# Kernel tuning notes

Hardware: AMD Instinct MI355X
Metric: run time of the kernel (lower is better)

The kernel has to match this reference:

```python
import jax, jax.numpy as jnp
import numpy as np

COMMITMENT_COST = 0.25
NUM_EMBEDDINGS = 512
EMBEDDING_DIM = 64


def setup_inputs() -> dict:
    key = jax.random.key(0)
    k1, k2 = jax.random.split(key)
    inputs = jax.random.normal(k1, (64, EMBEDDING_DIM, 32, 32), dtype=jnp.float32)
    # nn.Embedding init: uniform(-1/K, 1/K)
    emb_w = jax.random.uniform(
        k2, (NUM_EMBEDDINGS, EMBEDDING_DIM), dtype=jnp.float32,
        minval=-1.0 / NUM_EMBEDDINGS, maxval=1.0 / NUM_EMBEDDINGS)
    return {"inputs": inputs, "emb_w": emb_w}


def reference(inputs, emb_w):
    sg = jax.lax.stop_gradient
    # NCHW -> NHWC
    x = jnp.transpose(inputs, (0, 2, 3, 1))          # [B, H, W, D]
    B, H, W, D = x.shape
    flat = x.reshape(-1, D)                          # [N, D]
    dist = (jnp.sum(flat * flat, axis=1, keepdims=True)
            + jnp.sum(emb_w * emb_w, axis=1)
            - 2.0 * jnp.dot(flat, emb_w.T))          # [N, K]
    idx = jnp.argmin(dist, axis=1)                   # [N]
    # one-hot @ emb_w is just a gather
    quantized = emb_w[idx].reshape(B, H, W, D)       # [B, H, W, D]
    e_latent_loss = jnp.mean((sg(quantized) - x) ** 2)
    q_latent_loss = jnp.mean((quantized - sg(x)) ** 2)
    loss = q_latent_loss + COMMITMENT_COST * e_latent_loss
    # straight-through estimator
    quantized_st = x + sg(quantized - x)
    out = jnp.transpose(quantized_st, (0, 3, 1, 2))  # back to NCHW
    return loss, out, idx[:, None]
```

## Files before the change

### kernel.cpp

```cpp
#include <hip/hip_runtime.h>


#define D_    64
#define HW_   1024
#define N_    65536
#define K_    512
#define M_    128
#define CH_   128
#define NCH_  4
#define NDTOT (N_ * D_)

__global__ __launch_bounds__(256) void vq_norm_kernel(const float* __restrict__ emb,
                                                      float* __restrict__ wsn) {
    int k = blockIdx.x * 256 + threadIdx.x;
    if (k < K_) {
        const float* e = emb + k * D_;
        float r[8];
#pragma unroll
        for (int j = 0; j < 8; ++j) r[j] = __fmul_rn(e[j], e[j]);
#pragma unroll
        for (int i = 1; i < 8; ++i)
#pragma unroll
            for (int j = 0; j < 8; ++j)
                r[j] = __fadd_rn(r[j], __fmul_rn(e[i * 8 + j], e[i * 8 + j]));
        float s = __fadd_rn(__fadd_rn(__fadd_rn(r[0], r[1]), __fadd_rn(r[2], r[3])),
                            __fadd_rn(__fadd_rn(r[4], r[5]), __fadd_rn(r[6], r[7])));
        wsn[k] = s;
    }
}

__global__ __launch_bounds__(256, 2) void vq_main_kernel(const float* __restrict__ inp,
                                                         const float* __restrict__ emb,
                                                         const float* __restrict__ wsn,
                                                         float* __restrict__ out) {
    __shared__ float lds[16520];
    float* ldsx = lds;
    float* ldse = lds + 8192;
    float* sxs  = lds + 16384;
    float* partial = lds + 16512;

    const int tid = threadIdx.x;
    const int pg  = tid & 15;
    const int kg  = tid >> 4;
    const int n0  = blockIdx.x * M_;
    const int b   = n0 >> 10;
    const int hw0 = n0 & 1023;
    const float* xbase = inp + b * (D_ * HW_) + hw0;

#pragma unroll
    for (int i = 0; i < 8; ++i) {
        int q  = i * 256 + tid;
        int d  = q >> 5;
        int pq = q & 31;
        float4 v = *(const float4*)(xbase + d * HW_ + pq * 4);
        *(float4*)(ldsx + d * M_ + pq * 4) = v;
    }
    __syncthreads();

    if (tid < M_) {
        float r[8];
#pragma unroll
        for (int j = 0; j < 8; ++j) {
            float v = ldsx[j * M_ + tid];
            r[j] = __fmul_rn(v, v);
        }
#pragma unroll
        for (int i = 1; i < 8; ++i)
#pragma unroll
            for (int j = 0; j < 8; ++j) {
                float v = ldsx[(i * 8 + j) * M_ + tid];
                r[j] = __fadd_rn(r[j], __fmul_rn(v, v));
            }
        sxs[tid] = __fadd_rn(__fadd_rn(__fadd_rn(r[0], r[1]), __fadd_rn(r[2], r[3])),
                             __fadd_rn(__fadd_rn(r[4], r[5]), __fadd_rn(r[6], r[7])));
    }
    __syncthreads();

    float sxp[8];
#pragma unroll
    for (int pp = 0; pp < 8; ++pp) sxp[pp] = sxs[pg * 8 + pp];

    float runv[8];
    int   runi[8];
#pragma unroll
    for (int pp = 0; pp < 8; ++pp) { runv[pp] = 3.4e38f; runi[pp] = 0; }

    for (int c = 0; c < NCH_; ++c) {
        __syncthreads();
#pragma unroll
        for (int i = 0; i < 8; ++i) {
            int q  = i * 256 + tid;
            int kl = q & 127;
            int dq = q >> 7;
            float4 v = *(const float4*)(emb + (c * CH_ + kl) * D_ + dq * 4);
            ldse[(dq * 4 + 0) * CH_ + kl] = v.x;
            ldse[(dq * 4 + 1) * CH_ + kl] = v.y;
            ldse[(dq * 4 + 2) * CH_ + kl] = v.z;
            ldse[(dq * 4 + 3) * CH_ + kl] = v.w;
        }
        float4 nh0 = *(const float4*)(wsn + c * CH_ + kg * 8);
        float4 nh1 = *(const float4*)(wsn + c * CH_ + kg * 8 + 4);
        __syncthreads();

        float acc[8][8];
#pragma unroll
        for (int pp = 0; pp < 8; ++pp)
#pragma unroll
            for (int kk = 0; kk < 8; ++kk) acc[pp][kk] = 0.f;

#pragma unroll 2
        for (int d = 0; d < D_; ++d) {
            float4 xa = *(const float4*)(ldsx + d * M_ + pg * 8);
            float4 xb = *(const float4*)(ldsx + d * M_ + pg * 8 + 4);
            float4 ea = *(const float4*)(ldse + d * CH_ + kg * 8);
            float4 eb = *(const float4*)(ldse + d * CH_ + kg * 8 + 4);
            float xr[8] = {xa.x, xa.y, xa.z, xa.w, xb.x, xb.y, xb.z, xb.w};
            float er[8] = {ea.x, ea.y, ea.z, ea.w, eb.x, eb.y, eb.z, eb.w};
#pragma unroll
            for (int pp = 0; pp < 8; ++pp)
#pragma unroll
                for (int kk = 0; kk < 8; ++kk)
                    acc[pp][kk] = fmaf(xr[pp], er[kk], acc[pp][kk]);
        }

        float nk[8] = {nh0.x, nh0.y, nh0.z, nh0.w, nh1.x, nh1.y, nh1.z, nh1.w};
#pragma unroll
        for (int pp = 0; pp < 8; ++pp) {
            float sx = sxp[pp];
#pragma unroll
            for (int kk = 0; kk < 8; ++kk) {
                float t1 = __fadd_rn(sx, nk[kk]);
                float v  = __fadd_rn(t1, -2.0f * acc[pp][kk]);
                if (v < runv[pp]) { runv[pp] = v; runi[pp] = c * CH_ + kg * 8 + kk; }
            }
        }
    }

    __syncthreads();
    float* sv = ldse;
    int*   si = (int*)(ldse + 2048);
    int*   fi = (int*)(ldse + 4096);
#pragma unroll
    for (int pp = 0; pp < 8; ++pp) {
        sv[kg * M_ + pg * 8 + pp] = runv[pp];
        si[kg * M_ + pg * 8 + pp] = runi[pp];
    }
    __syncthreads();
    if (tid < M_) {
        float bv = 3.4e38f; int bi = 0x7fffffff;
#pragma unroll
        for (int g = 0; g < 16; ++g) {
            float v  = sv[g * M_ + tid];
            int   ii = si[g * M_ + tid];
            if (v < bv || (v == bv && ii < bi)) { bv = v; bi = ii; }
        }
        fi[tid] = bi;
        out[1 + NDTOT + n0 + tid] = (float)bi;
    }
    __syncthreads();

    float* obase = out + 1 + b * (D_ * HW_) + hw0;
    float local = 0.f;
    for (int i = 0; i < 32; ++i) {
        int q = i * 256 + tid;
        int d = q >> 7;
        int p = q & 127;
        int idx = fi[p];
        float e  = emb[idx * D_ + d];
        float xv = ldsx[d * M_ + p];
        float df = e - xv;
        local = fmaf(df, df, local);
        obase[d * HW_ + p] = e;
    }
#pragma unroll
    for (int off = 32; off > 0; off >>= 1)
        local += __shfl_down(local, off, 64);
    if ((tid & 63) == 0) partial[tid >> 6] = local;
    __syncthreads();
    if (tid == 0) {
        float t = partial[0] + partial[1] + partial[2] + partial[3];
        atomicAdd(out, t * (1.25f / (float)NDTOT));
    }
}

extern "C" void kernel_launch(void* const* d_in, const int* in_sizes, int n_in,
                              void* d_out, int out_size, void* d_ws, size_t ws_size,
                              hipStream_t stream) {
    const float* inp = (const float*)d_in[0];
    const float* emb = (const float*)d_in[1];
    float* out = (float*)d_out;
    float* wsn = (float*)d_ws;

    hipMemsetAsync(d_out, 0, sizeof(float), stream);
    vq_norm_kernel<<<2, 256, 0, stream>>>(emb, wsn);
    vq_main_kernel<<<512, 256, 0, stream>>>(inp, emb, wsn, out);
}
```

Before: 131.9 us.

## Fuse codebook norm into main kernel and hold pixel vectors in registers

Removes the separate norm kernel; each block now computes all codebook norms into LDS itself. The distance computation is restructured so each thread keeps two full 64-dim pixel vectors in registers and streams codebook rows directly from global memory (wave-uniform addresses), with each wave covering a quarter of the codebook. This drops the LDS staging and transpose of codebook chunks and the extra launch, at the cost of much lower per-load FMA reuse, redundant norm work per block, and high register pressure.

```diff
diff --git a/kernel.cpp b/kernel.cpp
--- a/kernel.cpp
+++ b/kernel.cpp
@@ -6,45 +6,24 @@
 #define N_    65536
 #define K_    512
 #define M_    128
-#define CH_   128
-#define NCH_  4
 #define NDTOT (N_ * D_)
 
-__global__ __launch_bounds__(256) void vq_norm_kernel(const float* __restrict__ emb,
-                                                      float* __restrict__ wsn) {
-    int k = blockIdx.x * 256 + threadIdx.x;
-    if (k < K_) {
-        const float* e = emb + k * D_;
-        float r[8];
-#pragma unroll
-        for (int j = 0; j < 8; ++j) r[j] = __fmul_rn(e[j], e[j]);
-#pragma unroll
-        for (int i = 1; i < 8; ++i)
-#pragma unroll
-            for (int j = 0; j < 8; ++j)
-                r[j] = __fadd_rn(r[j], __fmul_rn(e[i * 8 + j], e[i * 8 + j]));
-        float s = __fadd_rn(__fadd_rn(__fadd_rn(r[0], r[1]), __fadd_rn(r[2], r[3])),
-                            __fadd_rn(__fadd_rn(r[4], r[5]), __fadd_rn(r[6], r[7])));
-        wsn[k] = s;
-    }
-}
+__global__ __launch_bounds__(256, 2) void vq_fused_kernel(const float* __restrict__ inp,
+                                                          const float* __restrict__ emb,
+                                                          float* __restrict__ out) {
+    __shared__ float ldsx[D_ * M_];
+    __shared__ float ldsn[K_];
+    __shared__ float sv[4 * M_];
+    __shared__ int   si[4 * M_];
+    __shared__ int   fi[M_];
+    __shared__ float partial[4];
 
-__global__ __launch_bounds__(256, 2) void vq_main_kernel(const float* __restrict__ inp,
-                                                         const float* __restrict__ emb,
-                                                         const float* __restrict__ wsn,
-                                                         float* __restrict__ out) {
-    __shared__ float lds[16520];
-    float* ldsx = lds;
-    float* ldse = lds + 8192;
-    float* sxs  = lds + 16384;
-    float* partial = lds + 16512;
-
-    const int tid = threadIdx.x;
-    const int pg  = tid & 15;
-    const int kg  = tid >> 4;
-    const int n0  = blockIdx.x * M_;
-    const int b   = n0 >> 10;
-    const int hw0 = n0 & 1023;
+    const int tid  = threadIdx.x;
+    const int lane = tid & 63;
+    const int w    = tid >> 6;
+    const int n0   = blockIdx.x * M_;
+    const int b    = n0 >> 10;
+    const int hw0  = n0 & 1023;
     const float* xbase = inp + b * (D_ * HW_) + hw0;
 
 #pragma unroll
@@ -55,101 +34,91 @@
         float4 v = *(const float4*)(xbase + d * HW_ + pq * 4);
         *(float4*)(ldsx + d * M_ + pq * 4) = v;
     }
-    __syncthreads();
 
-    if (tid < M_) {
+#pragma unroll
+    for (int c = 0; c < 2; ++c) {
+        const int k = c * 256 + tid;
+        const float* e = emb + k * D_;
+        float el[64];
+#pragma unroll
+        for (int q = 0; q < 16; ++q) {
+            float4 v = *(const float4*)(e + q * 4);
+            el[4 * q + 0] = v.x; el[4 * q + 1] = v.y;
+            el[4 * q + 2] = v.z; el[4 * q + 3] = v.w;
+        }
         float r[8];
 #pragma unroll
-        for (int j = 0; j < 8; ++j) {
-            float v = ldsx[j * M_ + tid];
-            r[j] = __fmul_rn(v, v);
-        }
+        for (int j = 0; j < 8; ++j) r[j] = __fmul_rn(el[j], el[j]);
 #pragma unroll
         for (int i = 1; i < 8; ++i)
 #pragma unroll
-            for (int j = 0; j < 8; ++j) {
-                float v = ldsx[(i * 8 + j) * M_ + tid];
-                r[j] = __fadd_rn(r[j], __fmul_rn(v, v));
-            }
-        sxs[tid] = __fadd_rn(__fadd_rn(__fadd_rn(r[0], r[1]), __fadd_rn(r[2], r[3])),
-                             __fadd_rn(__fadd_rn(r[4], r[5]), __fadd_rn(r[6], r[7])));
+            for (int j = 0; j < 8; ++j)
+                r[j] = __fadd_rn(r[j], __fmul_rn(el[i * 8 + j], el[i * 8 + j]));
+        ldsn[k] = __fadd_rn(__fadd_rn(__fadd_rn(r[0], r[1]), __fadd_rn(r[2], r[3])),
+                            __fadd_rn(__fadd_rn(r[4], r[5]), __fadd_rn(r[6], r[7])));
     }
     __syncthreads();
 
-    float sxp[8];
+    float x0[64], x1[64];
 #pragma unroll
-    for (int pp = 0; pp < 8; ++pp) sxp[pp] = sxs[pg * 8 + pp];
-
-    float runv[8];
-    int   runi[8];
-#pragma unroll
-    for (int pp = 0; pp < 8; ++pp) { runv[pp] = 3.4e38f; runi[pp] = 0; }
-
-    for (int c = 0; c < NCH_; ++c) {
-        __syncthreads();
-#pragma unroll
-        for (int i = 0; i < 8; ++i) {
-            int q  = i * 256 + tid;
-            int kl = q & 127;
-            int dq = q >> 7;
-            float4 v = *(const float4*)(emb + (c * CH_ + kl) * D_ + dq * 4);
-            ldse[(dq * 4 + 0) * CH_ + kl] = v.x;
-            ldse[(dq * 4 + 1) * CH_ + kl] = v.y;
-            ldse[(dq * 4 + 2) * CH_ + kl] = v.z;
-            ldse[(dq * 4 + 3) * CH_ + kl] = v.w;
-        }
-        float4 nh0 = *(const float4*)(wsn + c * CH_ + kg * 8);
-        float4 nh1 = *(const float4*)(wsn + c * CH_ + kg * 8 + 4);
-        __syncthreads();
-
-        float acc[8][8];
-#pragma unroll
-        for (int pp = 0; pp < 8; ++pp)
-#pragma unroll
-            for (int kk = 0; kk < 8; ++kk) acc[pp][kk] = 0.f;
-
-#pragma unroll 2
-        for (int d = 0; d < D_; ++d) {
-            float4 xa = *(const float4*)(ldsx + d * M_ + pg * 8);
-            float4 xb = *(const float4*)(ldsx + d * M_ + pg * 8 + 4);
-            float4 ea = *(const float4*)(ldse + d * CH_ + kg * 8);
-            float4 eb = *(const float4*)(ldse + d * CH_ + kg * 8 + 4);
-            float xr[8] = {xa.x, xa.y, xa.z, xa.w, xb.x, xb.y, xb.z, xb.w};
-            float er[8] = {ea.x, ea.y, ea.z, ea.w, eb.x, eb.y, eb.z, eb.w};
-#pragma unroll
-            for (int pp = 0; pp < 8; ++pp)
-#pragma unroll
-                for (int kk = 0; kk < 8; ++kk)
-                    acc[pp][kk] = fmaf(xr[pp], er[kk], acc[pp][kk]);
-        }
-
-        float nk[8] = {nh0.x, nh0.y, nh0.z, nh0.w, nh1.x, nh1.y, nh1.z, nh1.w};
-#pragma unroll
-        for (int pp = 0; pp < 8; ++pp) {
-            float sx = sxp[pp];
-#pragma unroll
-            for (int kk = 0; kk < 8; ++kk) {
-                float t1 = __fadd_rn(sx, nk[kk]);
-                float v  = __fadd_rn(t1, -2.0f * acc[pp][kk]);
-                if (v < runv[pp]) { runv[pp] = v; runi[pp] = c * CH_ + kg * 8 + kk; }
-            }
-        }
+    for (int d = 0; d < 64; ++d) {
+        float2 v = *(const float2*)(ldsx + d * M_ + 2 * lane);
+        x0[d] = v.x; x1[d] = v.y;
     }
 
-    __syncthreads();
-    float* sv = ldse;
-    int*   si = (int*)(ldse + 2048);
-    int*   fi = (int*)(ldse + 4096);
+    float r0[8], r1[8];
 #pragma unroll
-    for (int pp = 0; pp < 8; ++pp) {
-        sv[kg * M_ + pg * 8 + pp] = runv[pp];
-        si[kg * M_ + pg * 8 + pp] = runi[pp];
+    for (int j = 0; j < 8; ++j) {
+        r0[j] = __fmul_rn(x0[j], x0[j]);
+        r1[j] = __fmul_rn(x1[j], x1[j]);
+    }
+#pragma unroll
+    for (int i = 1; i < 8; ++i)
+#pragma unroll
+        for (int j = 0; j < 8; ++j) {
+            r0[j] = __fadd_rn(r0[j], __fmul_rn(x0[i * 8 + j], x0[i * 8 + j]));
+            r1[j] = __fadd_rn(r1[j], __fmul_rn(x1[i * 8 + j], x1[i * 8 + j]));
+        }
+    const float sx0 = __fadd_rn(__fadd_rn(__fadd_rn(r0[0], r0[1]), __fadd_rn(r0[2], r0[3])),
+                                __fadd_rn(__fadd_rn(r0[4], r0[5]), __fadd_rn(r0[6], r0[7])));
+    const float sx1 = __fadd_rn(__fadd_rn(__fadd_rn(r1[0], r1[1]), __fadd_rn(r1[2], r1[3])),
+                                __fadd_rn(__fadd_rn(r1[4], r1[5]), __fadd_rn(r1[6], r1[7])));
+
+    float runv0 = 3.4e38f, runv1 = 3.4e38f;
+    int   runi0 = 0,       runi1 = 0;
+    const int k0 = w << 7;
+    const float* ew = emb + k0 * D_;
+#pragma unroll 2
+    for (int kk = 0; kk < 128; ++kk) {
+        const float* ek = ew + kk * D_;
+        const float nk = ldsn[k0 + kk];
+        float acc0 = 0.f, acc1 = 0.f;
+#pragma unroll
+        for (int q = 0; q < 16; ++q) {
+            float4 ev = *(const float4*)(ek + q * 4);
+            acc0 = fmaf(x0[4 * q + 0], ev.x, acc0); acc1 = fmaf(x1[4 * q + 0], ev.x, acc1);
+            acc0 = fmaf(x0[4 * q + 1], ev.y, acc0); acc1 = fmaf(x1[4 * q + 1], ev.y, acc1);
+            acc0 = fmaf(x0[4 * q + 2], ev.z, acc0); acc1 = fmaf(x1[4 * q + 2], ev.z, acc1);
+            acc0 = fmaf(x0[4 * q + 3], ev.w, acc0); acc1 = fmaf(x1[4 * q + 3], ev.w, acc1);
+        }
+        float t0 = __fadd_rn(sx0, nk);
+        float v0 = __fadd_rn(t0, -2.0f * acc0);
+        if (v0 < runv0) { runv0 = v0; runi0 = k0 + kk; }
+        float t1 = __fadd_rn(sx1, nk);
+        float v1 = __fadd_rn(t1, -2.0f * acc1);
+        if (v1 < runv1) { runv1 = v1; runi1 = k0 + kk; }
+    }
+
+    {
+        const int p0 = 2 * lane, p1 = 2 * lane + 1;
+        sv[w * M_ + p0] = runv0; si[w * M_ + p0] = runi0;
+        sv[w * M_ + p1] = runv1; si[w * M_ + p1] = runi1;
     }
     __syncthreads();
     if (tid < M_) {
         float bv = 3.4e38f; int bi = 0x7fffffff;
 #pragma unroll
-        for (int g = 0; g < 16; ++g) {
+        for (int g = 0; g < 4; ++g) {
             float v  = sv[g * M_ + tid];
             int   ii = si[g * M_ + tid];
             if (v < bv || (v == bv && ii < bi)) { bv = v; bi = ii; }
@@ -189,9 +158,8 @@
     const float* inp = (const float*)d_in[0];
     const float* emb = (const float*)d_in[1];
     float* out = (float*)d_out;
-    float* wsn = (float*)d_ws;
+    (void)d_ws; (void)ws_size;
 
     hipMemsetAsync(d_out, 0, sizeof(float), stream);
-    vq_norm_kernel<<<2, 256, 0, stream>>>(emb, wsn);
-    vq_main_kernel<<<512, 256, 0, stream>>>(inp, emb, wsn, out);
+    vq_fused_kernel<<<512, 256, 0, stream>>>(inp, emb, out);
 }
```

Measured after the change: 202.9 us. +53.9%, slower.
